# Optimization experiments

Measured on AMD Instinct MI355X. Metric: run time of the kernel, lower is better.

Reference implementation:

```python
import jax, jax.numpy as jnp
import numpy as np

N = 3072          # num nodes
E = 49152         # num edges (avg degree 16)
D = 256           # hidden_dim
O = 512           # output_dim
H = 8             # num_heads
DH = D // H       # head_dim = 32
NET = 5           # num_edge_types
NC = 8            # num_communities
L_LOC = 2         # num_local_layers
L_GLB = 2         # num_global_layers


def _layernorm(x, g, b, eps=1e-5):
    m = jnp.mean(x, axis=-1, keepdims=True)
    v = jnp.mean((x - m) ** 2, axis=-1, keepdims=True)
    return (x - m) * jax.lax.rsqrt(v + eps) * g + b


def setup_inputs() -> dict:
    key = jax.random.key(0)
    ks = jax.random.split(key, 40)
    s = 0.02
    inp = {
        "x": jax.random.normal(ks[0], (N, 1), jnp.float32),
        "edge_index": jax.random.randint(ks[1], (2, E), 0, N),
        "edge_types": jax.random.randint(ks[2], (E,), 0, NET),
        "pos_encoding": jax.random.normal(ks[3], (N, D), jnp.float32),
        "community_ids": jax.random.randint(ks[4], (N,), 0, NC),
        "adj_matrix": jnp.zeros((N, N), jnp.float32),
        # node embedding Linear(1, D)
        "emb_w": jax.random.normal(ks[5], (1, D)) * s,
        "emb_b": jnp.zeros((D,)),
        # local (Graphormer) layers, stacked over L_LOC
        "loc_qw": jax.random.normal(ks[6], (L_LOC, D, D)) * s,
        "loc_qb": jnp.zeros((L_LOC, D)),
        "loc_kw": jax.random.normal(ks[7], (L_LOC, D, D)) * s,
        "loc_kb": jnp.zeros((L_LOC, D)),
        "loc_vw": jax.random.normal(ks[8], (L_LOC, D, D)) * s,
        "loc_vb": jnp.zeros((L_LOC, D)),
        "loc_ow": jax.random.normal(ks[9], (L_LOC, D, D)) * s,
        "loc_ob": jnp.zeros((L_LOC, D)),
        "loc_eb": jax.random.normal(ks[10], (L_LOC, NET, H)) * s,  # edge-type attn bias per head
        "loc_ln_g": jnp.ones((L_LOC, D)),
        "loc_ln_b": jnp.zeros((L_LOC, D)),
        # global interaction layers, stacked over L_GLB
        "glob_qw": jax.random.normal(ks[11], (L_GLB, D, D)) * s,
        "glob_qb": jnp.zeros((L_GLB, D)),
        "glob_kw": jax.random.normal(ks[12], (L_GLB, D, D)) * s,
        "glob_kb": jnp.zeros((L_GLB, D)),
        "glob_vw": jax.random.normal(ks[13], (L_GLB, D, D)) * s,
        "glob_vb": jnp.zeros((L_GLB, D)),
        "glob_ow": jax.random.normal(ks[14], (L_GLB, D, D)) * s,
        "glob_ob": jnp.zeros((L_GLB, D)),
        "glob_ln_g": jnp.ones((L_GLB, D)),
        "glob_ln_b": jnp.zeros((L_GLB, D)),
        # output projection
        "out_w": jax.random.normal(ks[15], (D, O)) * s,
        "out_b": jnp.zeros((O,)),
    }
    return inp


def reference(x, edge_index, edge_types, pos_encoding, community_ids, adj_matrix,
              emb_w, emb_b,
              loc_qw, loc_qb, loc_kw, loc_kb, loc_vw, loc_vb, loc_ow, loc_ob,
              loc_eb, loc_ln_g, loc_ln_b,
              glob_qw, glob_qb, glob_kw, glob_kb, glob_vw, glob_vb,
              glob_ow, glob_ob, glob_ln_g, glob_ln_b,
              out_w, out_b):
    n = x.shape[0]
    h = x @ emb_w + emb_b                                  # [N, D]
    same = community_ids[:, None] == community_ids[None, :]  # [N, N] same-community mask
    src, dst = edge_index[0], edge_index[1]

    # Local layers: the original per-community subgraph loop (with full attention
    # inside each community) is mathematically a single masked full attention
    # restricted to same-community pairs, with edge-type bias at graph edges.
    for l in range(loc_qw.shape[0]):
        hp = h + pos_encoding
        q = (hp @ loc_qw[l] + loc_qb[l]).reshape(n, H, DH)
        k = (hp @ loc_kw[l] + loc_kb[l]).reshape(n, H, DH)
        v = (hp @ loc_vw[l] + loc_vb[l]).reshape(n, H, DH)
        # edge-type attention bias, scattered at edges  -> [H, N, N]
        bias = jnp.zeros((H, n, n), dtype=h.dtype).at[:, src, dst].add(loc_eb[l][edge_types].T)
        scores = jnp.einsum('nhd,mhd->hnm', q, k) / np.sqrt(DH) + bias
        scores = jnp.where(same[None, :, :], scores, -jnp.inf)  # attend within community only
        attn = jax.nn.softmax(scores, axis=-1)
        o = jnp.einsum('hnm,mhd->nhd', attn, v).reshape(n, D)
        h = _layernorm(h + o @ loc_ow[l] + loc_ob[l], loc_ln_g[l], loc_ln_b[l])

    # Global interaction: attend only to nodes in *different* communities
    for g in range(glob_qw.shape[0]):
        Q = h @ glob_qw[g] + glob_qb[g]
        K = h @ glob_kw[g] + glob_kb[g]
        V = h @ glob_vw[g] + glob_vb[g]
        scores = (Q @ K.T) / np.sqrt(DH)                   # scaled by head_dim as in source
        scores = jnp.where(~same, scores, -jnp.inf)        # mask same-community (incl. self)
        attn = jax.nn.softmax(scores, axis=-1)
        o = (attn @ V) @ glob_ow[g] + glob_ob[g]
        h = _layernorm(o + h, glob_ln_g[g], glob_ln_b[g])

    return h @ out_w + out_b                               # [N, O]
```

## Files before the change

### kernel.cpp

```cpp
#include <hip/hip_runtime.h>
#include <hip/hip_bf16.h>
#include <stdint.h>

#define NN 3072
#define EE 49152
#define DD 256
#define OO 512
#define HH 8
#define DHH 32
#define NETT 5
#define NC 8
#define NCMAX 512
#define SCP 516
#define KS 24
#define NW 17

typedef __attribute__((ext_vector_type(8))) short short8;
typedef __attribute__((ext_vector_type(4))) float f32x4;

__device__ __forceinline__ short f2bf_s(float f){
    __hip_bfloat16 h = __float2bfloat16(f);
    return *reinterpret_cast<short*>(&h);
}
__device__ __forceinline__ float bf2f_s(short v){
    __hip_bfloat16 h;
    *reinterpret_cast<short*>(&h) = v;
    return __bfloat162float(h);
}

__global__ void k_embed(const float* __restrict__ x, const float* __restrict__ w,
                        const float* __restrict__ b, const float* __restrict__ pos,
                        float* __restrict__ h, short* __restrict__ hbf, short* __restrict__ hpbf){
    int i = blockIdx.x * 256 + threadIdx.x;
    int n = i >> 8, d = i & 255;
    float v = x[n] * w[d] + b[d];
    h[i] = v;
    hbf[i] = f2bf_s(v);
    hpbf[i] = f2bf_s(v + pos[i]);
}

__global__ __launch_bounds__(256) void k_vtrans(const float* __restrict__ v, short* __restrict__ vt){
    __shared__ float t[32][33];
    int bx = blockIdx.x;
    int by = blockIdx.y;
    int lx = threadIdx.x & 31, ly = threadIdx.x >> 5;
    for (int i = ly; i < 32; i += 8)
        t[i][lx] = v[(size_t)(bx * 32 + i) * DD + by * 32 + lx];
    __syncthreads();
    for (int r = ly; r < 32; r += 8)
        vt[(size_t)(by * 32 + r) * NN + bx * 32 + lx] = f2bf_s(t[lx][r]);
}

__global__ __launch_bounds__(256) void k_vtrans_sorted(const float* __restrict__ v,
                                                       const int* __restrict__ perm,
                                                       short* __restrict__ vt){
    __shared__ float t[32][33];
    int bx = blockIdx.x;
    int by = blockIdx.y;
    int lx = threadIdx.x & 31, ly = threadIdx.x >> 5;
    for (int i = ly; i < 32; i += 8)
        t[i][lx] = v[(size_t)perm[bx * 32 + i] * DD + by * 32 + lx];
    __syncthreads();
    for (int r = ly; r < 32; r += 8)
        vt[(size_t)(by * 32 + r) * NN + bx * 32 + lx] = f2bf_s(t[lx][r]);
}

struct WT {
    const float* src[NW];
    short*       dst[NW];
    int          M[NW];
};
__global__ __launch_bounds__(256) void k_wtrans(WT wt){
    int id = blockIdx.z;
    int M = wt.M[id];
    int bx = blockIdx.x;
    if (bx * 32 >= M) return;
    int by = blockIdx.y;
    __shared__ float t[32][33];
    int lx = threadIdx.x & 31, ly = threadIdx.x >> 5;
    const float* w = wt.src[id];
    for (int i = ly; i < 32; i += 8)
        t[i][lx] = w[(size_t)(by * 32 + i) * M + bx * 32 + lx];
    __syncthreads();
    short* d = wt.dst[id];
    for (int r = ly; r < 32; r += 8)
        d[(size_t)(bx * 32 + r) * DD + by * 32 + lx] = f2bf_s(t[lx][r]);
}

__global__ void k_count(const int* __restrict__ ei, int* __restrict__ cnt){
    int e = blockIdx.x * 256 + threadIdx.x;
    if (e < EE) atomicAdd(&cnt[ei[e]], 1);
}

__global__ void k_scan(const int* __restrict__ cnt, int* __restrict__ rp){
    __shared__ int part[256];
    int tid = threadIdx.x;
    int base = tid * 12;
    int loc[12]; int s = 0;
    for (int i = 0; i < 12; i++){ loc[i] = s; s += cnt[base + i]; }
    part[tid] = s; __syncthreads();
    if (tid == 0){ int a = 0; for (int i = 0; i < 256; i++){ int t = part[i]; part[i] = a; a += t; } }
    __syncthreads();
    int b = part[tid];
    for (int i = 0; i < 12; i++) rp[base + i] = b + loc[i];
    if (tid == 255) rp[NN] = b + s;
}

__global__ void k_fill(const int* __restrict__ ei, const int* __restrict__ et,
                       const int* __restrict__ rp, int* __restrict__ cur,
                       int* __restrict__ e_dst, int* __restrict__ e_typ){
    int e = blockIdx.x * 256 + threadIdx.x;
    if (e < EE){
        int s = ei[e], d = ei[EE + e];
        int p = atomicAdd(&cur[s], 1);
        int idx = rp[s] + p;
        e_dst[idx] = d; e_typ[idx] = et[e];
    }
}

__global__ void k_ccount(const int* __restrict__ comm, int* __restrict__ ccnt){
    int n = blockIdx.x * 256 + threadIdx.x;
    if (n < NN) atomicAdd(&ccnt[comm[n]], 1);
}

__global__ void k_cscan(const int* __restrict__ ccnt, int* __restrict__ cstart){
    cstart[0] = 0;
    for (int c = 0; c < NC; c++) cstart[c + 1] = cstart[c] + ccnt[c];
}

__global__ void k_cfill(const int* __restrict__ comm, const int* __restrict__ cstart,
                        int* __restrict__ ccur, int* __restrict__ perm, int* __restrict__ inv){
    int n = blockIdx.x * 256 + threadIdx.x;
    if (n < NN){
        int c = comm[n];
        int p = cstart[c] + atomicAdd(&ccur[c], 1);
        perm[p] = n; inv[n] = p;
    }
}

template<int M>
__global__ __launch_bounds__(256) void k_gemm_mfma(
        const short* __restrict__ A, const short* __restrict__ Wt,
        const float* __restrict__ bias, float* __restrict__ C){
    int tid = threadIdx.x;
    int w = tid >> 6, lane = tid & 63, quad = lane >> 4, col = lane & 15;
    int m0 = blockIdx.x * 64 + w * 16;
    int n0 = blockIdx.y * 64;

    const short* arow = A + (size_t)(m0 + col) * DD;

    f32x4 acc[4];
    #pragma unroll
    for (int su = 0; su < 4; su++) acc[su] = (f32x4){0.f, 0.f, 0.f, 0.f};

    #pragma unroll
    for (int f = 0; f < 8; f++){
        int k0 = f * 32 + quad * 8;
        short8 af = *(const short8*)(arow + k0);
        #pragma unroll
        for (int su = 0; su < 4; su++){
            short8 bf = *(const short8*)(Wt + (size_t)(n0 + su * 16 + col) * DD + k0);
            acc[su] = __builtin_amdgcn_mfma_f32_16x16x32_bf16(af, bf, acc[su], 0, 0, 0);
        }
    }

    #pragma unroll
    for (int su = 0; su < 4; su++){
        int n = n0 + su * 16 + col;
        float bz = bias[n];
        #pragma unroll
        for (int r = 0; r < 4; r++)
            C[(size_t)(m0 + quad * 4 + r) * M + n] = acc[su][r] + bz;
    }
}

struct QKV {
    const short* Wt[3];
    const float* bias[3];
    float*       Cf[3];
    short*       Cb[3];
};
__global__ __launch_bounds__(256) void k_gemm_qkv(
        const short* __restrict__ A, QKV q, const int* __restrict__ inv){
    int z = blockIdx.z;
    const short* Wt = q.Wt[z];
    const float* bias = q.bias[z];
    float* Cf = q.Cf[z];
    short* Cb = q.Cb[z];

    int tid = threadIdx.x;
    int w = tid >> 6, lane = tid & 63, quad = lane >> 4, col = lane & 15;
    int m0 = blockIdx.x * 64 + w * 16;
    int n0 = blockIdx.y * 64;

    const short* arow = A + (size_t)(m0 + col) * DD;

    f32x4 acc[4];
    #pragma unroll
    for (int su = 0; su < 4; su++) acc[su] = (f32x4){0.f, 0.f, 0.f, 0.f};

    #pragma unroll
    for (int f = 0; f < 8; f++){
        int k0 = f * 32 + quad * 8;
        short8 af = *(const short8*)(arow + k0);
        #pragma unroll
        for (int su = 0; su < 4; su++){
            short8 bf = *(const short8*)(Wt + (size_t)(n0 + su * 16 + col) * DD + k0);
            acc[su] = __builtin_amdgcn_mfma_f32_16x16x32_bf16(af, bf, acc[su], 0, 0, 0);
        }
    }

    #pragma unroll
    for (int su = 0; su < 4; su++){
        int n = n0 + su * 16 + col;
        float bz = bias[n];
        #pragma unroll
        for (int r = 0; r < 4; r++){
            float val = acc[su][r] + bz;
            int m = m0 + quad * 4 + r;
            if (Cf) Cf[(size_t)m * DD + n] = val;
            if (Cb){
                int ms = inv ? inv[m] : m;
                Cb[(size_t)ms * DD + n] = f2bf_s(val);
            }
        }
    }
}

__global__ __launch_bounds__(256) void k_gemm_o_ln(
        const short* __restrict__ A, const short* __restrict__ Wt,
        const float* __restrict__ bias,
        const float* __restrict__ g, const float* __restrict__ b,
        const float* __restrict__ pos,
        float* __restrict__ h, short* __restrict__ hbf, short* __restrict__ hpbf){
    __shared__ float t[16][258];
    int tid = threadIdx.x;
    int w = tid >> 6, lane = tid & 63, quad = lane >> 4, col = lane & 15;
    int m0 = blockIdx.x * 16;
    int n0 = w * 64;

    const short* arow = A + (size_t)(m0 + col) * DD;

    f32x4 acc[4];
    #pragma unroll
    for (int su = 0; su < 4; su++) acc[su] = (f32x4){0.f, 0.f, 0.f, 0.f};

    #pragma unroll
    for (int f = 0; f < 8; f++){
        int k0 = f * 32 + quad * 8;
        short8 af = *(const short8*)(arow + k0);
        #pragma unroll
        for (int su = 0; su < 4; su++){
            short8 bf = *(const short8*)(Wt + (size_t)(n0 + su * 16 + col) * DD + k0);
            acc[su] = __builtin_amdgcn_mfma_f32_16x16x32_bf16(af, bf, acc[su], 0, 0, 0);
        }
    }

    #pragma unroll
    for (int su = 0; su < 4; su++){
        int n = n0 + su * 16 + col;
        float bz = bias[n];
        #pragma unroll
        for (int r = 0; r < 4; r++)
            t[quad * 4 + r][n] = acc[su][r] + bz;
    }
    __syncthreads();

    int row = tid >> 4, l16 = tid & 15;
    int m = m0 + row;
    float v[16];
    float s = 0.f;
    #pragma unroll
    for (int j = 0; j < 16; j++){
        int d = l16 + j * 16;
        float vv = t[row][d] + h[(size_t)m * DD + d];
        v[j] = vv; s += vv;
    }
    #pragma unroll
    for (int off = 1; off < 16; off <<= 1) s += __shfl_xor(s, off);
    float mean = s * (1.0f / 256.0f);
    float s2 = 0.f;
    #pragma unroll
    for (int j = 0; j < 16; j++){ float c = v[j] - mean; s2 += c * c; }
    #pragma unroll
    for (int off = 1; off < 16; off <<= 1) s2 += __shfl_xor(s2, off);
    float rstd = rsqrtf(s2 * (1.0f / 256.0f) + 1e-5f);
    #pragma unroll
    for (int j = 0; j < 16; j++){
        int d = l16 + j * 16;
        float out = (v[j] - mean) * rstd * g[d] + b[d];
        size_t idx = (size_t)m * DD + d;
        h[idx] = out;
        hbf[idx] = f2bf_s(out);
        if (pos) hpbf[idx] = f2bf_s(out + pos[idx]);
    }
}

__global__ __launch_bounds__(256) void k_local_attn6(
        const short* __restrict__ Qs, const short* __restrict__ Ks, const short* __restrict__ Vts,
        const int* __restrict__ cstart, const int* __restrict__ perm, const int* __restrict__ inv,
        const int* __restrict__ rp, const int* __restrict__ e_dst, const int* __restrict__ e_typ,
        const float* __restrict__ eb, short* __restrict__ obbf){
    int c  = blockIdx.y;
    int hh = blockIdx.z;
    int cs0 = cstart[c], cs1 = cstart[c + 1];
    int Nc = cs1 - cs0;
    int p0 = blockIdx.x * 16;
    if (p0 >= Nc) return;
    int tid = threadIdx.x;
    int w = tid >> 6, lane = tid & 63, quad = lane >> 4, col = lane & 15;
    int nt  = (Nc + 15) >> 4;
    int nt2 = (Nc + 31) >> 5;

    __shared__ float sc[16][SCP];
    __shared__ float linv[16];
    __shared__ int qnode[16];

    if (tid < 16) qnode[tid] = (p0 + tid < Nc) ? perm[cs0 + p0 + tid] : -1;

    int qrow = cs0 + min(p0 + col, Nc - 1);
    short8 qf = *(const short8*)(Qs + (size_t)qrow * DD + hh * DHH + quad * 8);

    const float scale = 0.17677669529663687f;

    for (int t = w; t < nt; t += 4){
        int kt = t * 16;
        int krow = cs0 + min(kt + col, Nc - 1);
        short8 kf = *(const short8*)(Ks + (size_t)krow * DD + hh * DHH + quad * 8);
        f32x4 s = __builtin_amdgcn_mfma_f32_16x16x32_bf16(qf, kf, (f32x4){0.f,0.f,0.f,0.f}, 0, 0, 0);
        #pragma unroll
        for (int r = 0; r < 4; r++)
            sc[quad * 4 + r][kt + col] = s[r] * scale;
    }
    __syncthreads();

    int qi = tid >> 4, l16 = tid & 15;
    {
        int n = qnode[qi];
        if (n >= 0){
            int re = rp[n + 1];
            for (int e2 = rp[n] + l16; e2 < re; e2 += 16){
                int dpos = inv[e_dst[e2]];
                if (dpos >= cs0 && dpos < cs1)
                    atomicAdd(&sc[qi][dpos - cs0], eb[e_typ[e2] * HH + hh]);
            }
        }
    }
    __syncthreads();

    {
        float lm = -1e30f;
        for (int m = l16; m < Nc; m += 16) lm = fmaxf(lm, sc[qi][m]);
        #pragma unroll
        for (int off = 1; off < 16; off <<= 1) lm = fmaxf(lm, __shfl_xor(lm, off));
        float ls = 0.f;
        for (int m = l16; m < Nc; m += 16){
            float e_ = __expf(sc[qi][m] - lm);
            sc[qi][m] = e_;
            ls += e_;
        }
        for (int m = (Nc & ~15) + l16; m < nt2 * 32; m += 16)
            if (m >= Nc) sc[qi][m] = 0.f;
        #pragma unroll
        for (int off = 1; off < 16; off <<= 1) ls += __shfl_xor(ls, off);
        if (l16 == 0) linv[qi] = 1.f / ls;
    }
    __syncthreads();

    f32x4 acc0 = (f32x4){0.f,0.f,0.f,0.f}, acc1 = (f32x4){0.f,0.f,0.f,0.f};
    for (int t2 = w; t2 < nt2; t2 += 4){
        int kt = t2 * 32;
        float4 pa = *(const float4*)&sc[col][kt + quad * 8];
        float4 pb = *(const float4*)&sc[col][kt + quad * 8 + 4];
        short8 pf;
        pf[0] = f2bf_s(pa.x); pf[1] = f2bf_s(pa.y); pf[2] = f2bf_s(pa.z); pf[3] = f2bf_s(pa.w);
        pf[4] = f2bf_s(pb.x); pf[5] = f2bf_s(pb.y); pf[6] = f2bf_s(pb.z); pf[7] = f2bf_s(pb.w);
        const short* vb0 = Vts + (size_t)(hh * DHH + col) * NN + cs0 + kt + quad * 8;
        short8 vf0 = *(const short8*)(vb0);
        short8 vf1 = *(const short8*)(vb0 + (size_t)16 * NN);
        acc0 = __builtin_amdgcn_mfma_f32_16x16x32_bf16(pf, vf0, acc0, 0, 0, 0);
        acc1 = __builtin_amdgcn_mfma_f32_16x16x32_bf16(pf, vf1, acc1, 0, 0, 0);
    }
    __syncthreads();
    {
        float (*pv)[16][33] = reinterpret_cast<float (*)[16][33]>(&sc[0][0]);
        #pragma unroll
        for (int r = 0; r < 4; r++){
            pv[w][quad * 4 + r][col]      = acc0[r];
            pv[w][quad * 4 + r][col + 16] = acc1[r];
        }
        __syncthreads();

        int q = tid >> 4, d0 = tid & 15;
        int n = qnode[q];
        #pragma unroll
        for (int half = 0; half < 2; half++){
            int dd = d0 + half * 16;
            float sum = pv[0][q][dd] + pv[1][q][dd] + pv[2][q][dd] + pv[3][q][dd];
            if (n >= 0) obbf[(size_t)n * DD + hh * DHH + dd] = f2bf_s(sum * linv[q]);
        }
    }
}

__device__ __forceinline__ int kl_addr(int row, int ks){
    return row * 256 + (ks ^ ((row & 7) << 3));
}
__device__ __forceinline__ int vl_addr(int d, int ks){
    return d * 32 + (ks ^ (((d >> 1) & 3) << 3));
}
__device__ __forceinline__ int pl_addr(int w, int row, int k){
    return w * 512 + row * 32 + ((k & 24) ^ (((row >> 1) & 3) << 3)) + (k & 7);
}
__global__ __launch_bounds__(256) void k_glob_mfma11(
        const short* __restrict__ Qb, const short* __restrict__ Kb,
        const short* __restrict__ Vt, const int* __restrict__ comm,
        short* __restrict__ Opart, float* __restrict__ lpart){
    int tid = threadIdx.x;
    int w = tid >> 6, lane = tid & 63, quad = lane >> 4, col = lane & 15;
    int qt = blockIdx.x * 64 + w * 16;
    int split = blockIdx.y;
    int ks0 = split * (NN / KS);
    const int NT = NN / KS / 32;

    __shared__ __align__(16) short Kl[32 * 256];
    __shared__ __align__(16) short Vl[256 * 32];
    __shared__ __align__(16) short Pl[4 * 16 * 32];

    short8 qf[8];
    #pragma unroll
    for (int f = 0; f < 8; f++)
        qf[f] = *(const short8*)(Qb + (size_t)(qt + col) * DD + f * 32 + quad * 8);

    int qc[4];
    #pragma unroll
    for (int r = 0; r < 4; r++) qc[r] = comm[qt + quad * 4 + r];

    f32x4 accO[16];
    #pragma unroll
    for (int dt = 0; dt < 16; dt++) accO[dt] = (f32x4){0.f, 0.f, 0.f, 0.f};
    float l_[4] = {0.f, 0.f, 0.f, 0.f};

    const float scale = 0.17677669529663687f;

    int ksg = tid & 31;
    int kr0 = tid >> 5;
    int vsg = tid & 3;
    int vd0 = tid >> 2;

    short8 kpre[4], vpre[4];
    #pragma unroll
    for (int i = 0; i < 4; i++){
        kpre[i] = *(const short8*)(Kb + (size_t)(ks0 + kr0 + 8 * i) * DD + ksg * 8);
        vpre[i] = *(const short8*)(Vt + (size_t)(vd0 + 64 * i) * NN + ks0 + vsg * 8);
    }

    for (int t = 0; t < NT; t++){
        int kt = ks0 + t * 32;
        __syncthreads();
        #pragma unroll
        for (int i = 0; i < 4; i++){
            *(short8*)&Kl[kl_addr(kr0 + 8 * i, ksg * 8)] = kpre[i];
            *(short8*)&Vl[vl_addr(vd0 + 64 * i, vsg * 8)] = vpre[i];
        }
        __syncthreads();
        if (t + 1 < NT){
            int kn = kt + 32;
            #pragma unroll
            for (int i = 0; i < 4; i++){
                kpre[i] = *(const short8*)(Kb + (size_t)(kn + kr0 + 8 * i) * DD + ksg * 8);
                vpre[i] = *(const short8*)(Vt + (size_t)(vd0 + 64 * i) * NN + kn + vsg * 8);
            }
        }

        f32x4 s0 = (f32x4){0.f,0.f,0.f,0.f}, s1 = (f32x4){0.f,0.f,0.f,0.f};
        #pragma unroll
        for (int f = 0; f < 8; f++){
            int ko = f * 32 + quad * 8;
            short8 kf0 = *(const short8*)&Kl[kl_addr(col, ko)];
            short8 kf1 = *(const short8*)&Kl[kl_addr(16 + col, ko)];
            s0 = __builtin_amdgcn_mfma_f32_16x16x32_bf16(qf[f], kf0, s0, 0, 0, 0);
            s1 = __builtin_amdgcn_mfma_f32_16x16x32_bf16(qf[f], kf1, s1, 0, 0, 0);
        }

        int cm0 = comm[kt + col], cm1 = comm[kt + 16 + col];
        #pragma unroll
        for (int r = 0; r < 4; r++){
            float p0 = (cm0 != qc[r]) ? __expf(s0[r] * scale) : 0.f;
            float p1 = (cm1 != qc[r]) ? __expf(s1[r] * scale) : 0.f;
            l_[r] += p0 + p1;
            int row = quad * 4 + r;
            Pl[pl_addr(w, row, col)]      = f2bf_s(p0);
            Pl[pl_addr(w, row, col + 16)] = f2bf_s(p1);
        }
        short8 pf = *(const short8*)&Pl[pl_addr(w, col, quad * 8)];
        #pragma unroll
        for (int dt = 0; dt < 16; dt++){
            short8 vf = *(const short8*)&Vl[vl_addr(dt * 16 + col, quad * 8)];
            accO[dt] = __builtin_amdgcn_mfma_f32_16x16x32_bf16(pf, vf, accO[dt], 0, 0, 0);
        }
    }

    #pragma unroll
    for (int r = 0; r < 4; r++){
        float vv = l_[r];
        #pragma unroll
        for (int off = 1; off < 16; off <<= 1) vv += __shfl_xor(vv, off);
        l_[r] = vv;
    }

    #pragma unroll
    for (int r = 0; r < 4; r++){
        int row = qt + quad * 4 + r;
        if (col == 0) lpart[split * NN + row] = l_[r];
        #pragma unroll
        for (int dt = 0; dt < 16; dt++)
            Opart[((size_t)split * NN + row) * DD + dt * 16 + col] = f2bf_s(accO[dt][r]);
    }
}

__global__ __launch_bounds__(256) void k_gmerge(
        const short* __restrict__ Opart, const float* __restrict__ lpart,
        short* __restrict__ obbf){
    int qn = blockIdx.x, d = threadIdx.x;
    float l = 0.f, val = 0.f;
    #pragma unroll
    for (int s = 0; s < KS; s++){
        l += lpart[s * NN + qn];
        val += bf2f_s(Opart[((size_t)s * NN + qn) * DD + d]);
    }
    obbf[(size_t)qn * DD + d] = f2bf_s(val / l);
}

extern "C" void kernel_launch(void* const* d_in, const int* in_sizes, int n_in,
                              void* d_out, int out_size, void* d_ws, size_t ws_size,
                              hipStream_t stream){
    const float* x        = (const float*)d_in[0];
    const int*   ei       = (const int*)  d_in[1];
    const int*   et       = (const int*)  d_in[2];
    const float* pos      = (const float*)d_in[3];
    const int*   comm     = (const int*)  d_in[4];
    const float* emb_w    = (const float*)d_in[6];
    const float* emb_b    = (const float*)d_in[7];
    const float* loc_qw   = (const float*)d_in[8];
    const float* loc_qb   = (const float*)d_in[9];
    const float* loc_kw   = (const float*)d_in[10];
    const float* loc_kb   = (const float*)d_in[11];
    const float* loc_vw   = (const float*)d_in[12];
    const float* loc_vb   = (const float*)d_in[13];
    const float* loc_ow   = (const float*)d_in[14];
    const float* loc_ob   = (const float*)d_in[15];
    const float* loc_eb   = (const float*)d_in[16];
    const float* loc_ln_g = (const float*)d_in[17];
    const float* loc_ln_b = (const float*)d_in[18];
    const float* glob_qw  = (const float*)d_in[19];
    const float* glob_qb  = (const float*)d_in[20];
    const float* glob_kw  = (const float*)d_in[21];
    const float* glob_kb  = (const float*)d_in[22];
    const float* glob_vw  = (const float*)d_in[23];
    const float* glob_vb  = (const float*)d_in[24];
    const float* glob_ow  = (const float*)d_in[25];
    const float* glob_ob  = (const float*)d_in[26];
    const float* glob_ln_g= (const float*)d_in[27];
    const float* glob_ln_b= (const float*)d_in[28];
    const float* out_w    = (const float*)d_in[29];
    const float* out_b    = (const float*)d_in[30];

    float* h    = (float*)d_ws;
    float* vb_  = h    + NN * DD;
    float* lpart= vb_  + NN * DD;
    int* cnt    = (int*)(lpart + KS * NN);
    int* cur    = cnt + NN;
    int* ccnt   = cur + NN;
    int* ccur   = ccnt + NC;
    int* cstart = ccur + NC;
    int* rp     = cstart + NC + 1;
    int* perm   = rp + NN + 1;
    int* inv    = perm + NN;
    int* e_dst  = inv + NN;
    int* e_typ  = e_dst + EE;
    short* Qbf  = (short*)(((uintptr_t)(e_typ + EE) + 15) & ~(uintptr_t)15);
    short* Kbf  = Qbf + NN * DD;
    short* Vt   = Kbf + NN * DD;
    short* WtAll= Vt + (size_t)DD * NN;
    short* Qs   = WtAll + 16 * DD * DD + DD * OO;
    short* Ks2  = Qs + (size_t)NN * DD;
    short* Vts  = Ks2 + (size_t)NN * DD;
    short* Opart= Vts + (size_t)DD * NN;
    short* hbf  = Opart + (size_t)KS * NN * DD;
    short* hpbf = hbf + (size_t)NN * DD;
    short* obbf = hpbf + (size_t)NN * DD;

    WT wt;
    const float* wsrc[NW] = {
        loc_qw, loc_kw, loc_vw, loc_ow,
        loc_qw + DD * DD, loc_kw + DD * DD, loc_vw + DD * DD, loc_ow + DD * DD,
        glob_qw, glob_kw, glob_vw, glob_ow,
        glob_qw + DD * DD, glob_kw + DD * DD, glob_vw + DD * DD, glob_ow + DD * DD,
        out_w };
    for (int i = 0; i < NW; i++){
        wt.src[i] = wsrc[i];
        wt.dst[i] = WtAll + (size_t)i * DD * DD;
        wt.M[i]   = (i == 16) ? OO : DD;
    }
    short* WtLQ[2] = { WtAll + 0 * DD * DD, WtAll + 4 * DD * DD };
    short* WtLK[2] = { WtAll + 1 * DD * DD, WtAll + 5 * DD * DD };
    short* WtLV[2] = { WtAll + 2 * DD * DD, WtAll + 6 * DD * DD };
    short* WtLO[2] = { WtAll + 3 * DD * DD, WtAll + 7 * DD * DD };
    short* WtGQ[2] = { WtAll + 8 * DD * DD, WtAll + 12 * DD * DD };
    short* WtGK[2] = { WtAll + 9 * DD * DD, WtAll + 13 * DD * DD };
    short* WtGV[2] = { WtAll + 10 * DD * DD, WtAll + 14 * DD * DD };
    short* WtGO[2] = { WtAll + 11 * DD * DD, WtAll + 15 * DD * DD };
    short* WtOut   = WtAll + 16 * DD * DD;

    (void)hipMemsetAsync(cnt, 0, sizeof(int) * (2 * NN + 2 * NC), stream);

    k_embed<<<NN * DD / 256, 256, 0, stream>>>(x, emb_w, emb_b, pos, h, hbf, hpbf);
    k_wtrans<<<dim3(16, 8, NW), 256, 0, stream>>>(wt);
    k_count<<<EE / 256, 256, 0, stream>>>(ei, cnt);
    k_scan<<<1, 256, 0, stream>>>(cnt, rp);
    k_fill<<<EE / 256, 256, 0, stream>>>(ei, et, rp, cur, e_dst, e_typ);
    k_ccount<<<NN / 256, 256, 0, stream>>>(comm, ccnt);
    k_cscan<<<1, 1, 0, stream>>>(ccnt, cstart);
    k_cfill<<<NN / 256, 256, 0, stream>>>(comm, cstart, ccur, perm, inv);

    for (int l = 0; l < 2; l++){
        QKV q;
        q.Wt[0] = WtLQ[l]; q.Wt[1] = WtLK[l]; q.Wt[2] = WtLV[l];
        q.bias[0] = loc_qb + l * DD; q.bias[1] = loc_kb + l * DD; q.bias[2] = loc_vb + l * DD;
        q.Cf[0] = nullptr; q.Cf[1] = nullptr; q.Cf[2] = vb_;
        q.Cb[0] = Qs; q.Cb[1] = Ks2; q.Cb[2] = nullptr;
        k_gemm_qkv<<<dim3(NN / 64, DD / 64, 3), 256, 0, stream>>>(hpbf, q, inv);
        k_vtrans_sorted<<<dim3(NN / 32, DD / 32), 256, 0, stream>>>(vb_, perm, Vts);
        k_local_attn6<<<dim3(NCMAX / 16, NC, HH), 256, 0, stream>>>(
            Qs, Ks2, Vts, cstart, perm, inv, rp, e_dst, e_typ,
            loc_eb + l * NETT * HH, obbf);
        k_gemm_o_ln<<<NN / 16, 256, 0, stream>>>(
            obbf, WtLO[l], loc_ob + l * DD, loc_ln_g + l * DD, loc_ln_b + l * DD,
            (l == 0) ? pos : nullptr, h, hbf, hpbf);
    }

    for (int g = 0; g < 2; g++){
        QKV q;
        q.Wt[0] = WtGQ[g]; q.Wt[1] = WtGK[g]; q.Wt[2] = WtGV[g];
        q.bias[0] = glob_qb + g * DD; q.bias[1] = glob_kb + g * DD; q.bias[2] = glob_vb + g * DD;
        q.Cf[0] = nullptr; q.Cf[1] = nullptr; q.Cf[2] = vb_;
        q.Cb[0] = Qbf; q.Cb[1] = Kbf; q.Cb[2] = nullptr;
        k_gemm_qkv<<<dim3(NN / 64, DD / 64, 3), 256, 0, stream>>>(hbf, q, nullptr);
        k_vtrans<<<dim3(NN / 32, DD / 32), 256, 0, stream>>>(vb_, Vt);
        k_glob_mfma11<<<dim3(NN / 64, KS), 256, 0, stream>>>(Qbf, Kbf, Vt, comm, Opart, lpart);
        k_gmerge<<<NN, 256, 0, stream>>>(Opart, lpart, obbf);
        k_gemm_o_ln<<<NN / 16, 256, 0, stream>>>(
            obbf, WtGO[g], glob_ob + g * DD, glob_ln_g + g * DD, glob_ln_b + g * DD,
            nullptr, h, hbf, nullptr);
    }

    k_gemm_mfma<OO><<<dim3(NN / 64, OO / 64), 256, 0, stream>>>(hbf, WtOut, out_b, (float*)d_out);
}
```

Measured before the change: 510.3 us.

## Fuse V transpose into QKV GEMM epilogue and retune global attention split

The QKV GEMM now writes V directly in transposed bf16 layout, gathering input rows through the sort permutation instead of scattering outputs via the inverse permutation. This removes the separate fp32 V buffer and both transpose kernels. The global attention kernel drops V register prefetching in favour of direct loads, adds an occupancy launch bound, and uses a smaller key split (16 instead of 24). The lower split cuts merge work and partial-result traffic but exposes more of the V load latency.

```diff
diff --git a/kernel.cpp b/kernel.cpp
--- a/kernel.cpp
+++ b/kernel.cpp
@@ -12,10 +12,11 @@
 #define NC 8
 #define NCMAX 512
 #define SCP 516
-#define KS 24
+#define KS 16
 #define NW 17
 
 typedef __attribute__((ext_vector_type(8))) short short8;
+typedef __attribute__((ext_vector_type(4))) short short4v;
 typedef __attribute__((ext_vector_type(4))) float f32x4;
 
 __device__ __forceinline__ short f2bf_s(float f){
@@ -37,32 +38,6 @@
     h[i] = v;
     hbf[i] = f2bf_s(v);
     hpbf[i] = f2bf_s(v + pos[i]);
-}
-
-__global__ __launch_bounds__(256) void k_vtrans(const float* __restrict__ v, short* __restrict__ vt){
-    __shared__ float t[32][33];
-    int bx = blockIdx.x;
-    int by = blockIdx.y;
-    int lx = threadIdx.x & 31, ly = threadIdx.x >> 5;
-    for (int i = ly; i < 32; i += 8)
-        t[i][lx] = v[(size_t)(bx * 32 + i) * DD + by * 32 + lx];
-    __syncthreads();
-    for (int r = ly; r < 32; r += 8)
-        vt[(size_t)(by * 32 + r) * NN + bx * 32 + lx] = f2bf_s(t[lx][r]);
-}
-
-__global__ __launch_bounds__(256) void k_vtrans_sorted(const float* __restrict__ v,
-                                                       const int* __restrict__ perm,
-                                                       short* __restrict__ vt){
-    __shared__ float t[32][33];
-    int bx = blockIdx.x;
-    int by = blockIdx.y;
-    int lx = threadIdx.x & 31, ly = threadIdx.x >> 5;
-    for (int i = ly; i < 32; i += 8)
-        t[i][lx] = v[(size_t)perm[bx * 32 + i] * DD + by * 32 + lx];
-    __syncthreads();
-    for (int r = ly; r < 32; r += 8)
-        vt[(size_t)(by * 32 + r) * NN + bx * 32 + lx] = f2bf_s(t[lx][r]);
 }
 
 struct WT {
@@ -177,23 +152,23 @@
 struct QKV {
     const short* Wt[3];
     const float* bias[3];
-    float*       Cf[3];
-    short*       Cb[3];
+    short*       Cb[2];
+    short*       VtOut;
 };
 __global__ __launch_bounds__(256) void k_gemm_qkv(
-        const short* __restrict__ A, QKV q, const int* __restrict__ inv){
+        const short* __restrict__ A, QKV q, const int* __restrict__ permRow){
     int z = blockIdx.z;
     const short* Wt = q.Wt[z];
     const float* bias = q.bias[z];
-    float* Cf = q.Cf[z];
-    short* Cb = q.Cb[z];
 
     int tid = threadIdx.x;
     int w = tid >> 6, lane = tid & 63, quad = lane >> 4, col = lane & 15;
     int m0 = blockIdx.x * 64 + w * 16;
     int n0 = blockIdx.y * 64;
 
-    const short* arow = A + (size_t)(m0 + col) * DD;
+    int arowIdx = m0 + col;
+    if (permRow) arowIdx = permRow[arowIdx];
+    const short* arow = A + (size_t)arowIdx * DD;
 
     f32x4 acc[4];
     #pragma unroll
@@ -210,19 +185,25 @@
         }
     }
 
-    #pragma unroll
-    for (int su = 0; su < 4; su++){
-        int n = n0 + su * 16 + col;
-        float bz = bias[n];
-        #pragma unroll
-        for (int r = 0; r < 4; r++){
-            float val = acc[su][r] + bz;
-            int m = m0 + quad * 4 + r;
-            if (Cf) Cf[(size_t)m * DD + n] = val;
-            if (Cb){
-                int ms = inv ? inv[m] : m;
-                Cb[(size_t)ms * DD + n] = f2bf_s(val);
-            }
+    if (z == 2){
+        #pragma unroll
+        for (int su = 0; su < 4; su++){
+            int n = n0 + su * 16 + col;
+            float bz = bias[n];
+            short4v pk;
+            #pragma unroll
+            for (int r = 0; r < 4; r++) pk[r] = f2bf_s(acc[su][r] + bz);
+            *(short4v*)(q.VtOut + (size_t)n * NN + m0 + quad * 4) = pk;
+        }
+    } else {
+        short* Cb = q.Cb[z];
+        #pragma unroll
+        for (int su = 0; su < 4; su++){
+            int n = n0 + su * 16 + col;
+            float bz = bias[n];
+            #pragma unroll
+            for (int r = 0; r < 4; r++)
+                Cb[(size_t)(m0 + quad * 4 + r) * DD + n] = f2bf_s(acc[su][r] + bz);
         }
     }
 }
@@ -411,7 +392,7 @@
 __device__ __forceinline__ int pl_addr(int w, int row, int k){
     return w * 512 + row * 32 + ((k & 24) ^ (((row >> 1) & 3) << 3)) + (k & 7);
 }
-__global__ __launch_bounds__(256) void k_glob_mfma11(
+__global__ __launch_bounds__(256, 4) void k_glob_mfma12(
         const short* __restrict__ Qb, const short* __restrict__ Kb,
         const short* __restrict__ Vt, const int* __restrict__ comm,
         short* __restrict__ Opart, float* __restrict__ lpart){
@@ -447,29 +428,28 @@
     int vsg = tid & 3;
     int vd0 = tid >> 2;
 
-    short8 kpre[4], vpre[4];
-    #pragma unroll
-    for (int i = 0; i < 4; i++){
+    short8 kpre[4];
+    #pragma unroll
+    for (int i = 0; i < 4; i++)
         kpre[i] = *(const short8*)(Kb + (size_t)(ks0 + kr0 + 8 * i) * DD + ksg * 8);
-        vpre[i] = *(const short8*)(Vt + (size_t)(vd0 + 64 * i) * NN + ks0 + vsg * 8);
-    }
 
     for (int t = 0; t < NT; t++){
         int kt = ks0 + t * 32;
         __syncthreads();
         #pragma unroll
+        for (int i = 0; i < 4; i++)
+            *(short8*)&Kl[kl_addr(kr0 + 8 * i, ksg * 8)] = kpre[i];
+        #pragma unroll
         for (int i = 0; i < 4; i++){
-            *(short8*)&Kl[kl_addr(kr0 + 8 * i, ksg * 8)] = kpre[i];
-            *(short8*)&Vl[vl_addr(vd0 + 64 * i, vsg * 8)] = vpre[i];
+            short8 vv = *(const short8*)(Vt + (size_t)(vd0 + 64 * i) * NN + kt + vsg * 8);
+            *(short8*)&Vl[vl_addr(vd0 + 64 * i, vsg * 8)] = vv;
         }
         __syncthreads();
         if (t + 1 < NT){
             int kn = kt + 32;
             #pragma unroll
-            for (int i = 0; i < 4; i++){
+            for (int i = 0; i < 4; i++)
                 kpre[i] = *(const short8*)(Kb + (size_t)(kn + kr0 + 8 * i) * DD + ksg * 8);
-                vpre[i] = *(const short8*)(Vt + (size_t)(vd0 + 64 * i) * NN + kn + vsg * 8);
-            }
         }
 
         f32x4 s0 = (f32x4){0.f,0.f,0.f,0.f}, s1 = (f32x4){0.f,0.f,0.f,0.f};
@@ -566,8 +546,7 @@
     const float* out_b    = (const float*)d_in[30];
 
     float* h    = (float*)d_ws;
-    float* vb_  = h    + NN * DD;
-    float* lpart= vb_  + NN * DD;
+    float* lpart= h + NN * DD;
     int* cnt    = (int*)(lpart + KS * NN);
     int* cur    = cnt + NN;
     int* ccnt   = cur + NN;
@@ -627,10 +606,9 @@
         QKV q;
         q.Wt[0] = WtLQ[l]; q.Wt[1] = WtLK[l]; q.Wt[2] = WtLV[l];
         q.bias[0] = loc_qb + l * DD; q.bias[1] = loc_kb + l * DD; q.bias[2] = loc_vb + l * DD;
-        q.Cf[0] = nullptr; q.Cf[1] = nullptr; q.Cf[2] = vb_;
-        q.Cb[0] = Qs; q.Cb[1] = Ks2; q.Cb[2] = nullptr;
-        k_gemm_qkv<<<dim3(NN / 64, DD / 64, 3), 256, 0, stream>>>(hpbf, q, inv);
-        k_vtrans_sorted<<<dim3(NN / 32, DD / 32), 256, 0, stream>>>(vb_, perm, Vts);
+        q.Cb[0] = Qs; q.Cb[1] = Ks2;
+        q.VtOut = Vts;
+        k_gemm_qkv<<<dim3(NN / 64, DD / 64, 3), 256, 0, stream>>>(hpbf, q, perm);
         k_local_attn6<<<dim3(NCMAX / 16, NC, HH), 256, 0, stream>>>(
             Qs, Ks2, Vts, cstart, perm, inv, rp, e_dst, e_typ,
             loc_eb + l * NETT * HH, obbf);
@@ -643,11 +621,10 @@
         QKV q;
         q.Wt[0] = WtGQ[g]; q.Wt[1] = WtGK[g]; q.Wt[2] = WtGV[g];
         q.bias[0] = glob_qb + g * DD; q.bias[1] = glob_kb + g * DD; q.bias[2] = glob_vb + g * DD;
-        q.Cf[0] = nullptr; q.Cf[1] = nullptr; q.Cf[2] = vb_;
-        q.Cb[0] = Qbf; q.Cb[1] = Kbf; q.Cb[2] = nullptr;
+        q.Cb[0] = Qbf; q.Cb[1] = Kbf;
+        q.VtOut = Vt;
         k_gemm_qkv<<<dim3(NN / 64, DD / 64, 3), 256, 0, stream>>>(hbf, q, nullptr);
-        k_vtrans<<<dim3(NN / 32, DD / 32), 256, 0, stream>>>(vb_, Vt);
-        k_glob_mfma11<<<dim3(NN / 64, KS), 256, 0, stream>>>(Qbf, Kbf, Vt, comm, Opart, lpart);
+        k_glob_mfma12<<<dim3(NN / 64, KS), 256, 0, stream>>>(Qbf, Kbf, Vt, comm, Opart, lpart);
         k_gmerge<<<NN, 256, 0, stream>>>(Opart, lpart, obbf);
         k_gemm_o_ln<<<NN / 16, 256, 0, stream>>>(
             obbf, WtGO[g], glob_ob + g * DD, glob_ln_g + g * DD, glob_ln_b + g * DD,
```

Measured after the change: 521.0 us. 2.1% more time.
